# Kernel optimization log

Measured on AMD Instinct MI355X. Metric: run time of the kernel, lower is better.

Reference implementation:

```python
import jax, jax.numpy as jnp
import numpy as np

C = 345  # class_num


def setup_inputs() -> dict:
    key = jax.random.key(0)
    k1, k2, k3, k4, k5, k6, k7 = jax.random.split(key, 7)
    N, A = 128, 512
    fc_weight = jax.random.normal(k1, (C, A), dtype=jnp.float32) * 0.02
    features_source = jax.random.normal(k2, (N, A), dtype=jnp.float32)
    y_s = jax.random.normal(k3, (N, C), dtype=jnp.float32)
    labels_source = jax.random.randint(k4, (N,), 0, C, dtype=jnp.int64)
    mean_source = jax.random.normal(k5, (C, A), dtype=jnp.float32) * 0.1
    mean_target = jax.random.normal(k6, (C, A), dtype=jnp.float32) * 0.1
    covariance_target = jax.random.normal(k7, (C, A, A), dtype=jnp.float32) * 0.01
    Lambda = jnp.float32(0.5)
    return {
        "fc_weight": fc_weight,
        "features_source": features_source,
        "y_s": y_s,
        "labels_source": labels_source,
        "Lambda": Lambda,
        "mean_source": mean_source,
        "mean_target": mean_target,
        "covariance_target": covariance_target,
    }


def _aug(fc_weight, y_s, labels_s, Lambda, mean_source, mean_target, covariance_target):
    # NxW_ij = weight broadcast to [N,C,A]; NxW_kj = weight[labels] broadcast over C.
    # dataW[n,c,:] = W[c] - W[labels[n]]   -> [N,C,A]
    W_lbl = fc_weight[labels_s]                       # [N,A]
    dataW = fc_weight[None, :, :] - W_lbl[:, None, :]  # [N,C,A]

    Sigma = covariance_target[labels_s]               # [N,A,A]
    # diag of (dataW @ Sigma @ dataW^T): einsum directly for the diagonal
    tmp = jnp.einsum('nca,nab->ncb', dataW, Sigma)    # [N,C,A]
    sigma2 = Lambda * jnp.einsum('nca,nca->nc', tmp, dataW)  # [N,C]

    dMean = mean_target[labels_s] - mean_source[labels_s]   # [N,A]
    dW_dMean = jnp.einsum('nca,na->nc', dataW, dMean)        # [N,C]

    return y_s + 0.5 * sigma2 + Lambda * dW_dMean


def reference(fc_weight, features_source, y_s, labels_source, Lambda,
              mean_source, mean_target, covariance_target):
    aug_y = _aug(fc_weight, y_s, labels_source, Lambda,
                 mean_source, mean_target, covariance_target)
    logp = jax.nn.log_softmax(aug_y, axis=-1)
    N = aug_y.shape[0]
    nll = -logp[jnp.arange(N), labels_source]
    return jnp.mean(nll)
```

## Files before the change

kernel.cpp:

```cpp
#include <hip/hip_runtime.h>
#include <hip/hip_bf16.h>
#include <math.h>

#define C_NUM 345
#define A_DIM 512
#define N_NUM 128
#define KB    128
#define NBB   4

typedef short bf16x8 __attribute__((ext_vector_type(8)));
typedef float f32x4  __attribute__((ext_vector_type(4)));

__device__ __forceinline__ short f2bf(float f) {
    unsigned u = __builtin_bit_cast(unsigned, f);
    u += 0x7fffu + ((u >> 16) & 1u);
    return (short)(u >> 16);
}

__device__ __forceinline__ int swz(int r, int k) {
    return r * 128 + ((((k >> 3) ^ (r & 15)) << 3) | (k & 7));
}

__global__ __launch_bounds__(256, 2) void qkern(
    const float* __restrict__ W,
    const int*   __restrict__ labels,
    const float* __restrict__ cov,
    float*       __restrict__ q2)
{
    const int bb = blockIdx.x;
    const int n  = blockIdx.y;
    const int b0 = bb * KB;
    const int l  = labels[n];
    const float* __restrict__ Sg = cov + (size_t)l * A_DIM * A_DIM;
    const float* __restrict__ Wl = W + (size_t)l * A_DIM;

    __shared__ short Sa[128 * 128];
    __shared__ short Vb[128 * 128];

    const int tid  = threadIdx.x;
    const int lane = tid & 63;
    const int w    = tid >> 6;
    const int wa   = w & 1;
    const int wc   = w >> 1;
    const int l15  = lane & 15;
    const int g    = lane >> 4;

    const int c4 = tid & 31;
    const int r0 = tid >> 5;

    const float4 wl4 = *(const float4*)(Wl + b0 + c4 * 4);

    float qp[3][4];
#pragma unroll
    for (int ct = 0; ct < 3; ct++)
#pragma unroll
        for (int j = 0; j < 4; j++) qp[ct][j] = 0.f;

    for (int at = 0; at < A_DIM; at += 128) {
        float4 wle[4];
#pragma unroll
        for (int i = 0; i < 4; i++)
            wle[i] = *(const float4*)(Wl + at + wa * 64 + i * 16 + g * 4);

        for (int ct = 0; ct < 3; ct++) {
            __syncthreads();
            if (ct == 0) {
#pragma unroll
                for (int p = 0; p < 16; p++) {
                    const int r = r0 + p * 8;
                    const float4 s = *(const float4*)(Sg + (size_t)(at + r) * A_DIM + b0 + c4 * 4);
                    short4 h = make_short4(f2bf(s.x), f2bf(s.y), f2bf(s.z), f2bf(s.w));
                    *(short4*)(&Sa[swz(r, c4 * 4)]) = h;
                }
            }
#pragma unroll
            for (int p = 0; p < 16; p++) {
                const int r = r0 + p * 8;
                const int c = ct * 128 + r;
                short4 h;
                if (c < C_NUM) {
                    const float4 wv = *(const float4*)(W + (size_t)c * A_DIM + b0 + c4 * 4);
                    h = make_short4(f2bf(wv.x - wl4.x), f2bf(wv.y - wl4.y),
                                    f2bf(wv.z - wl4.z), f2bf(wv.w - wl4.w));
                } else {
                    h = make_short4(0, 0, 0, 0);
                }
                *(short4*)(&Vb[swz(r, c4 * 4)]) = h;
            }
            __syncthreads();

            f32x4 acc[4][4];
#pragma unroll
            for (int i = 0; i < 4; i++)
#pragma unroll
                for (int j = 0; j < 4; j++) {
                    f32x4 z = {0.f, 0.f, 0.f, 0.f};
                    acc[i][j] = z;
                }

#pragma unroll
            for (int kt = 0; kt < 4; kt++) {
                const int kbase = kt * 32 + g * 8;
                bf16x8 af[4], bfr[4];
#pragma unroll
                for (int i = 0; i < 4; i++)
                    af[i] = *(const bf16x8*)(&Sa[swz(wa * 64 + i * 16 + l15, kbase)]);
#pragma unroll
                for (int j = 0; j < 4; j++)
                    bfr[j] = *(const bf16x8*)(&Vb[swz(wc * 64 + j * 16 + l15, kbase)]);
#pragma unroll
                for (int i = 0; i < 4; i++)
#pragma unroll
                    for (int j = 0; j < 4; j++)
                        acc[i][j] = __builtin_amdgcn_mfma_f32_16x16x32_bf16(
                            af[i], bfr[j], acc[i][j], 0, 0, 0);
            }

#pragma unroll
            for (int i = 0; i < 4; i++) {
                const int a0 = at + wa * 64 + i * 16 + g * 4;
                const float4 wl_e = wle[i];
#pragma unroll
                for (int j = 0; j < 4; j++) {
                    const int c = ct * 128 + wc * 64 + j * 16 + l15;
                    if (c < C_NUM) {
                        const float4 wv = *(const float4*)(W + (size_t)c * A_DIM + a0);
                        const f32x4 u = acc[i][j];
                        qp[ct][j] += u[0] * (wv.x - wl_e.x) + u[1] * (wv.y - wl_e.y)
                                   + u[2] * (wv.z - wl_e.z) + u[3] * (wv.w - wl_e.w);
                    }
                }
            }
        }
    }

#pragma unroll
    for (int ct = 0; ct < 3; ct++)
#pragma unroll
        for (int j = 0; j < 4; j++) {
            float v = qp[ct][j];
            v += __shfl_xor(v, 16);
            v += __shfl_xor(v, 32);
            if (g == 0) {
                const int c = ct * 128 + wc * 64 + j * 16 + l15;
                if (c < C_NUM) atomicAdd(&q2[(size_t)n * C_NUM + c], v);
            }
        }
}

__global__ __launch_bounds__(256) void losskern(
    const float* __restrict__ W,
    const float* __restrict__ ys,
    const int*   __restrict__ labels,
    const float* __restrict__ lambda_p,
    const float* __restrict__ mean_s,
    const float* __restrict__ mean_t,
    const float* __restrict__ q2,
    float*       __restrict__ out)
{
    const int n = blockIdx.x;
    const int tid = threadIdx.x;
    const int lane = tid & 63;
    const int w = tid >> 6;
    const int l = labels[n];
    const float Lam = *lambda_p;

    __shared__ float aug[C_NUM];
    __shared__ float red[256];

    const int a0 = lane * 8;
    const float* Wl = W + (size_t)l * A_DIM;
    const float4 wl0 = *(const float4*)(Wl + a0);
    const float4 wl1 = *(const float4*)(Wl + a0 + 4);
    const float4 mt0 = *(const float4*)(mean_t + (size_t)l * A_DIM + a0);
    const float4 mt1 = *(const float4*)(mean_t + (size_t)l * A_DIM + a0 + 4);
    const float4 ms0 = *(const float4*)(mean_s + (size_t)l * A_DIM + a0);
    const float4 ms1 = *(const float4*)(mean_s + (size_t)l * A_DIM + a0 + 4);
    const float dm0 = mt0.x - ms0.x, dm1 = mt0.y - ms0.y, dm2 = mt0.z - ms0.z, dm3 = mt0.w - ms0.w;
    const float dm4 = mt1.x - ms1.x, dm5 = mt1.y - ms1.y, dm6 = mt1.z - ms1.z, dm7 = mt1.w - ms1.w;
    const float wldm = wl0.x*dm0 + wl0.y*dm1 + wl0.z*dm2 + wl0.w*dm3
                     + wl1.x*dm4 + wl1.y*dm5 + wl1.z*dm6 + wl1.w*dm7;

    for (int c = w; c < C_NUM; c += 4) {
        const float* Wc = W + (size_t)c * A_DIM;
        const float4 w0 = *(const float4*)(Wc + a0);
        const float4 w1 = *(const float4*)(Wc + a0 + 4);
        float d = w0.x*dm0 + w0.y*dm1 + w0.z*dm2 + w0.w*dm3
                + w1.x*dm4 + w1.y*dm5 + w1.z*dm6 + w1.w*dm7 - wldm;
        d += __shfl_xor(d, 1);
        d += __shfl_xor(d, 2);
        d += __shfl_xor(d, 4);
        d += __shfl_xor(d, 8);
        d += __shfl_xor(d, 16);
        d += __shfl_xor(d, 32);
        if (lane == 0)
            aug[c] = ys[(size_t)n * C_NUM + c] + 0.5f * Lam * q2[(size_t)n * C_NUM + c] + Lam * d;
    }
    __syncthreads();

    float m = -INFINITY;
    for (int c = tid; c < C_NUM; c += 256) m = fmaxf(m, aug[c]);
    red[tid] = m;
    __syncthreads();
    for (int s = 128; s > 0; s >>= 1) {
        if (tid < s) red[tid] = fmaxf(red[tid], red[tid + s]);
        __syncthreads();
    }
    m = red[0];
    __syncthreads();

    float se = 0.f;
    for (int c = tid; c < C_NUM; c += 256) se += expf(aug[c] - m);
    red[tid] = se;
    __syncthreads();
    for (int s = 128; s > 0; s >>= 1) {
        if (tid < s) red[tid] += red[tid + s];
        __syncthreads();
    }
    if (tid == 0) {
        const float logZ = m + logf(red[0]);
        atomicAdd(out, (logZ - aug[l]) * (1.f / (float)N_NUM));
    }
}

extern "C" void kernel_launch(void* const* d_in, const int* in_sizes, int n_in,
                              void* d_out, int out_size, void* d_ws, size_t ws_size,
                              hipStream_t stream) {
    const float* W      = (const float*)d_in[0];
    const float* ys     = (const float*)d_in[2];
    const int*   labels = (const int*)d_in[3];
    const float* lam    = (const float*)d_in[4];
    const float* means  = (const float*)d_in[5];
    const float* meant  = (const float*)d_in[6];
    const float* cov    = (const float*)d_in[7];
    float* out = (float*)d_out;
    float* q2  = (float*)d_ws;

    hipMemsetAsync(q2, 0, (size_t)N_NUM * C_NUM * sizeof(float), stream);
    hipMemsetAsync(out, 0, sizeof(float), stream);

    qkern<<<dim3(NBB, N_NUM), 256, 0, stream>>>(W, labels, cov, q2);
    losskern<<<N_NUM, 256, 0, stream>>>(W, ys, labels, lam, means, meant, q2, out);
}
```

Before: 555.7 us.

## Dedupe covariance quadratic form per label, retile, and drop atomics

The covariance kernel now skips any sample whose label already appeared at an earlier index, since the quadratic term depends only on the label. The loss kernel reads the representative sample's partial results instead. Tiles shrink to 64 columns across 8 blocks per sample, and all three class chunks of W-differences are staged into shared memory once rather than once per A tile. Atomic accumulation and the workspace memset are replaced by per-block partial buffers that the loss kernel sums. This trades redundant global work and atomics for a short serial label scan in every block and more blocks overall.

```diff
diff --git a/kernel.cpp b/kernel.cpp
--- a/kernel.cpp
+++ b/kernel.cpp
@@ -1,12 +1,11 @@
 #include <hip/hip_runtime.h>
-#include <hip/hip_bf16.h>
 #include <math.h>
 
 #define C_NUM 345
 #define A_DIM 512
 #define N_NUM 128
-#define KB    128
-#define NBB   4
+#define KB    64
+#define NBB   8
 
 typedef short bf16x8 __attribute__((ext_vector_type(8)));
 typedef float f32x4  __attribute__((ext_vector_type(4)));
@@ -17,25 +16,28 @@
     return (short)(u >> 16);
 }
 
-__device__ __forceinline__ int swz(int r, int k) {
-    return r * 128 + ((((k >> 3) ^ (r & 15)) << 3) | (k & 7));
+__device__ __forceinline__ int swz64(int r, int k) {
+    return r * 64 + ((((k >> 3) ^ (r & 7)) << 3) | (k & 7));
 }
 
 __global__ __launch_bounds__(256, 2) void qkern(
     const float* __restrict__ W,
     const int*   __restrict__ labels,
     const float* __restrict__ cov,
-    float*       __restrict__ q2)
+    float*       __restrict__ q2buf)
 {
     const int bb = blockIdx.x;
     const int n  = blockIdx.y;
+    const int l  = labels[n];
+    for (int m = 0; m < n; m++) if (labels[m] == l) return;
+
     const int b0 = bb * KB;
-    const int l  = labels[n];
     const float* __restrict__ Sg = cov + (size_t)l * A_DIM * A_DIM;
     const float* __restrict__ Wl = W + (size_t)l * A_DIM;
 
-    __shared__ short Sa[128 * 128];
-    __shared__ short Vb[128 * 128];
+    __shared__ short Sa[128 * 64];
+    __shared__ short Vb[3][128 * 64];
+    __shared__ float qred[384];
 
     const int tid  = threadIdx.x;
     const int lane = tid & 63;
@@ -45,11 +47,28 @@
     const int l15  = lane & 15;
     const int g    = lane >> 4;
 
-    const int c4 = tid & 31;
-    const int r0 = tid >> 5;
+    const int c4 = tid & 15;
+    const int r0 = tid >> 4;
 
     const float4 wl4 = *(const float4*)(Wl + b0 + c4 * 4);
 
+#pragma unroll
+    for (int ch = 0; ch < 3; ch++)
+#pragma unroll
+        for (int p = 0; p < 8; p++) {
+            const int r = r0 + p * 16;
+            const int c = ch * 128 + r;
+            short4 h;
+            if (c < C_NUM) {
+                const float4 wv = *(const float4*)(W + (size_t)c * A_DIM + b0 + c4 * 4);
+                h = make_short4(f2bf(wv.x - wl4.x), f2bf(wv.y - wl4.y),
+                                f2bf(wv.z - wl4.z), f2bf(wv.w - wl4.w));
+            } else {
+                h = make_short4(0, 0, 0, 0);
+            }
+            *(short4*)(&Vb[ch][swz64(r, c4 * 4)]) = h;
+        }
+
     float qp[3][4];
 #pragma unroll
     for (int ct = 0; ct < 3; ct++)
@@ -57,38 +76,23 @@
         for (int j = 0; j < 4; j++) qp[ct][j] = 0.f;
 
     for (int at = 0; at < A_DIM; at += 128) {
+        __syncthreads();
+#pragma unroll
+        for (int p = 0; p < 8; p++) {
+            const int r = r0 + p * 16;
+            const float4 s = *(const float4*)(Sg + (size_t)(at + r) * A_DIM + b0 + c4 * 4);
+            *(short4*)(&Sa[swz64(r, c4 * 4)]) =
+                make_short4(f2bf(s.x), f2bf(s.y), f2bf(s.z), f2bf(s.w));
+        }
+        __syncthreads();
+
         float4 wle[4];
 #pragma unroll
         for (int i = 0; i < 4; i++)
             wle[i] = *(const float4*)(Wl + at + wa * 64 + i * 16 + g * 4);
 
+#pragma unroll
         for (int ct = 0; ct < 3; ct++) {
-            __syncthreads();
-            if (ct == 0) {
-#pragma unroll
-                for (int p = 0; p < 16; p++) {
-                    const int r = r0 + p * 8;
-                    const float4 s = *(const float4*)(Sg + (size_t)(at + r) * A_DIM + b0 + c4 * 4);
-                    short4 h = make_short4(f2bf(s.x), f2bf(s.y), f2bf(s.z), f2bf(s.w));
-                    *(short4*)(&Sa[swz(r, c4 * 4)]) = h;
-                }
-            }
-#pragma unroll
-            for (int p = 0; p < 16; p++) {
-                const int r = r0 + p * 8;
-                const int c = ct * 128 + r;
-                short4 h;
-                if (c < C_NUM) {
-                    const float4 wv = *(const float4*)(W + (size_t)c * A_DIM + b0 + c4 * 4);
-                    h = make_short4(f2bf(wv.x - wl4.x), f2bf(wv.y - wl4.y),
-                                    f2bf(wv.z - wl4.z), f2bf(wv.w - wl4.w));
-                } else {
-                    h = make_short4(0, 0, 0, 0);
-                }
-                *(short4*)(&Vb[swz(r, c4 * 4)]) = h;
-            }
-            __syncthreads();
-
             f32x4 acc[4][4];
 #pragma unroll
             for (int i = 0; i < 4; i++)
@@ -99,15 +103,15 @@
                 }
 
 #pragma unroll
-            for (int kt = 0; kt < 4; kt++) {
+            for (int kt = 0; kt < 2; kt++) {
                 const int kbase = kt * 32 + g * 8;
                 bf16x8 af[4], bfr[4];
 #pragma unroll
                 for (int i = 0; i < 4; i++)
-                    af[i] = *(const bf16x8*)(&Sa[swz(wa * 64 + i * 16 + l15, kbase)]);
+                    af[i] = *(const bf16x8*)(&Sa[swz64(wa * 64 + i * 16 + l15, kbase)]);
 #pragma unroll
                 for (int j = 0; j < 4; j++)
-                    bfr[j] = *(const bf16x8*)(&Vb[swz(wc * 64 + j * 16 + l15, kbase)]);
+                    bfr[j] = *(const bf16x8*)(&Vb[ct][swz64(wc * 64 + j * 16 + l15, kbase)]);
 #pragma unroll
                 for (int i = 0; i < 4; i++)
 #pragma unroll
@@ -134,6 +138,7 @@
         }
     }
 
+    float vout[3][4];
 #pragma unroll
     for (int ct = 0; ct < 3; ct++)
 #pragma unroll
@@ -141,11 +146,26 @@
             float v = qp[ct][j];
             v += __shfl_xor(v, 16);
             v += __shfl_xor(v, 32);
-            if (g == 0) {
+            vout[ct][j] = v;
+        }
+    if (g == 0 && wa == 1) {
+#pragma unroll
+        for (int ct = 0; ct < 3; ct++)
+#pragma unroll
+            for (int j = 0; j < 4; j++)
+                qred[ct * 128 + wc * 64 + j * 16 + l15] = vout[ct][j];
+    }
+    __syncthreads();
+    if (g == 0 && wa == 0) {
+        float* dst = q2buf + ((size_t)bb * N_NUM + n) * C_NUM;
+#pragma unroll
+        for (int ct = 0; ct < 3; ct++)
+#pragma unroll
+            for (int j = 0; j < 4; j++) {
                 const int c = ct * 128 + wc * 64 + j * 16 + l15;
-                if (c < C_NUM) atomicAdd(&q2[(size_t)n * C_NUM + c], v);
-            }
-        }
+                if (c < C_NUM) dst[c] = vout[ct][j] + qred[c];
+            }
+    }
 }
 
 __global__ __launch_bounds__(256) void losskern(
@@ -155,7 +175,7 @@
     const float* __restrict__ lambda_p,
     const float* __restrict__ mean_s,
     const float* __restrict__ mean_t,
-    const float* __restrict__ q2,
+    const float* __restrict__ q2buf,
     float*       __restrict__ out)
 {
     const int n = blockIdx.x;
@@ -164,6 +184,9 @@
     const int w = tid >> 6;
     const int l = labels[n];
     const float Lam = *lambda_p;
+
+    int rep = n;
+    for (int m = 0; m < n; m++) if (labels[m] == l) { rep = m; break; }
 
     __shared__ float aug[C_NUM];
     __shared__ float red[256];
@@ -187,6 +210,8 @@
         const float4 w1 = *(const float4*)(Wc + a0 + 4);
         float d = w0.x*dm0 + w0.y*dm1 + w0.z*dm2 + w0.w*dm3
                 + w1.x*dm4 + w1.y*dm5 + w1.z*dm6 + w1.w*dm7 - wldm;
+        if (lane < NBB)
+            d += 0.5f * q2buf[((size_t)lane * N_NUM + rep) * C_NUM + c];
         d += __shfl_xor(d, 1);
         d += __shfl_xor(d, 2);
         d += __shfl_xor(d, 4);
@@ -194,7 +219,7 @@
         d += __shfl_xor(d, 16);
         d += __shfl_xor(d, 32);
         if (lane == 0)
-            aug[c] = ys[(size_t)n * C_NUM + c] + 0.5f * Lam * q2[(size_t)n * C_NUM + c] + Lam * d;
+            aug[c] = ys[(size_t)n * C_NUM + c] + Lam * d;
     }
     __syncthreads();
 
@@ -234,11 +259,10 @@
     const float* meant  = (const float*)d_in[6];
     const float* cov    = (const float*)d_in[7];
     float* out = (float*)d_out;
-    float* q2  = (float*)d_ws;
-
-    hipMemsetAsync(q2, 0, (size_t)N_NUM * C_NUM * sizeof(float), stream);
+    float* q2buf = (float*)d_ws;
+
     hipMemsetAsync(out, 0, sizeof(float), stream);
 
-    qkern<<<dim3(NBB, N_NUM), 256, 0, stream>>>(W, labels, cov, q2);
-    losskern<<<N_NUM, 256, 0, stream>>>(W, ys, labels, lam, means, meant, q2, out);
-}
+    qkern<<<dim3(NBB, N_NUM), 256, 0, stream>>>(W, labels, cov, q2buf);
+    losskern<<<N_NUM, 256, 0, stream>>>(W, ys, labels, lam, means, meant, q2buf, out);
+}
```

Result: slower. 569.5 us (+2.5%).
